# Optimization experiments

Measured on AMD Instinct MI355X. Metric: run time of the kernel, lower is better.

Reference implementation:

```python
import jax, jax.numpy as jnp
import numpy as np

# Config constants (match init_kwargs)
E = 32          # num_experts
K = 4           # num_experts_per_token
G = 4           # num_expert_group
TG = 2          # topk_group
H = 2048        # hidden_size
F = 1024        # moe_intermediate_size
FS = 2048       # shared expert intermediate (moe_intermediate_size * num_shared_experts)
SCALE = 2.0     # routed_scaling_factor
B, S = 2, 1024
N = B * S
CAP = 2 * (N * K // E)


def setup_inputs() -> dict:
    key = jax.random.key(0)
    ks = jax.random.split(key, 9)
    w = 0.02  # init scale for weights
    return {
        "hidden_states": jax.random.normal(ks[0], (B, S, H), jnp.float32),
        "gate_w": jax.random.normal(ks[1], (E, H), jnp.float32) * w,
        "gate_bias": jax.random.normal(ks[2], (E,), jnp.float32) * w,
        "w1": jax.random.normal(ks[3], (E, H, F), jnp.float32) * w,
        "w2": jax.random.normal(ks[4], (E, F, H), jnp.float32) * w,
        "w3": jax.random.normal(ks[5], (E, H, F), jnp.float32) * w,
        "shared_gate": jax.random.normal(ks[6], (H, FS), jnp.float32) * w,
        "shared_up": jax.random.normal(ks[7], (H, FS), jnp.float32) * w,
        "shared_down": jax.random.normal(ks[8], (FS, H), jnp.float32) * w,
    }


def _gate(x, gate_w, gate_bias):
    # x: [N, H] -> (topk_idx [N,K] int32, topk_w [N,K] f32)
    logits = x @ gate_w.T                       # [N, E]
    scores = jax.nn.sigmoid(logits)
    sc = scores + gate_bias                     # scores_for_choice
    n = x.shape[0]
    grp = sc.reshape(n, G, E // G)
    group_scores = jax.lax.top_k(grp, 2)[0].sum(-1)          # [N, G]
    _, gidx = jax.lax.top_k(group_scores, TG)                # [N, TG]
    gmask = jnp.zeros((n, G), sc.dtype).at[jnp.arange(n)[:, None], gidx].set(1.0)
    smask = jnp.repeat(gmask, E // G, axis=1)                # [N, E]
    tmp = jnp.where(smask > 0, sc, 0.0)
    _, topk_idx = jax.lax.top_k(tmp, K)                      # [N, K]
    topk_w = jnp.take_along_axis(scores, topk_idx, axis=1)
    topk_w = topk_w / (topk_w.sum(-1, keepdims=True) + 1e-20)  # renormalize (K>1)
    return topk_idx, topk_w * SCALE


def _moe(x, topk_idx, topk_w, w1, w2, w3):
    # Capacity-based dispatch -> grouped SwiGLU GEMMs -> weighted combine.
    n = x.shape[0]
    flat_e = topk_idx.reshape(-1)                            # [N*K]
    oh = jax.nn.one_hot(flat_e, E, dtype=jnp.int32)
    pos = (jnp.cumsum(oh, axis=0) * oh).sum(-1) - 1          # slot within expert
    keep = pos < CAP
    slot = jnp.where(keep, pos, CAP)                         # CAP -> dropped via mode='drop'
    x_rep = jnp.repeat(x, K, axis=0)                         # [N*K, H]
    buf = jnp.zeros((E, CAP, H), x.dtype).at[flat_e, slot].set(x_rep, mode='drop')
    h = jax.nn.silu(jnp.einsum('ech,ehf->ecf', buf, w1)) * jnp.einsum('ech,ehf->ecf', buf, w3)
    ob = jnp.einsum('ecf,efh->ech', h, w2)                   # [E, CAP, H]
    y = ob[flat_e, jnp.minimum(slot, CAP - 1)]               # [N*K, H]
    y = jnp.where(keep[:, None], y, 0.0)
    return (y.reshape(n, K, H) * topk_w[:, :, None]).sum(1)  # [N, H]


def reference(hidden_states, gate_w, gate_bias, w1, w2, w3, shared_gate, shared_up, shared_down):
    b, s, h = hidden_states.shape
    x = hidden_states.reshape(-1, h)
    topk_idx, topk_w = _gate(x, gate_w, gate_bias)
    out = _moe(x, topk_idx, topk_w, w1, w2, w3)
    shared = (jax.nn.silu(x @ shared_gate) * (x @ shared_up)) @ shared_down
    return (out + shared).reshape(b, s, h)
```

## Files before the change

### kernel.cpp

```cpp
#include <hip/hip_runtime.h>
#include <stdint.h>
#include <math.h>

#define NTOK 2048
#define HDIM 2048
#define FDIM 1024
#define NEXP 32
#define TOPK 4
#define NGRP 4
#define CAP  512

typedef _Float16 f16;
typedef _Float16 half8 __attribute__((ext_vector_type(8)));
typedef _Float16 half2v __attribute__((ext_vector_type(2)));
typedef float f32x4 __attribute__((ext_vector_type(4)));

__device__ __forceinline__ int swz3(int n) { return (n ^ (n >> 2)) & 3; }

__device__ __forceinline__ int expert_off(const int* __restrict__ cnt, int e) {
  int s = 0;
  for (int i = 0; i < e; i++) s += cnt[i];
  return s;
}

__global__ __launch_bounds__(256) void gateconv_kernel(const float* __restrict__ x,
                                                       const float* __restrict__ gw,
                                                       const float* __restrict__ gb,
                                                       int* __restrict__ tidx,
                                                       float* __restrict__ tw,
                                                       f16* __restrict__ xbt) {
  int t = blockIdx.x;
  int tid = threadIdx.x;
  int e = tid >> 3, p = tid & 7;
  const f32x4* xr = (const f32x4*)(x + (size_t)t * HDIM);
  const f32x4* wr = (const f32x4*)(gw + (size_t)e * HDIM);
  float s = 0.f;
  for (int c = 0; c < 64; c++) {
    f32x4 a = xr[p + c * 8], w = wr[p + c * 8];
    s += a[0] * w[0] + a[1] * w[1] + a[2] * w[2] + a[3] * w[3];
  }
  s += __shfl_down(s, 4, 8);
  s += __shfl_down(s, 2, 8);
  s += __shfl_down(s, 1, 8);
  __shared__ float lg[NEXP];
  if (p == 0) lg[e] = s;

  {
    int c8 = tid * 8;
    const float* pp = x + (size_t)t * HDIM + c8;
    f32x4 a = *(const f32x4*)pp;
    f32x4 b = *(const f32x4*)(pp + 4);
    half8 v;
    v[0] = (f16)a[0]; v[1] = (f16)a[1]; v[2] = (f16)a[2]; v[3] = (f16)a[3];
    v[4] = (f16)b[0]; v[5] = (f16)b[1]; v[6] = (f16)b[2]; v[7] = (f16)b[3];
    *(half8*)((char*)xbt + (size_t)(c8 >> 5) * 131072 + t * 64 + (c8 & 31) * 2) = v;
  }

  __syncthreads();
  if (tid == 0) {
    float sc[NEXP], scb[NEXP];
    for (int i = 0; i < NEXP; i++) {
      sc[i] = 1.f / (1.f + expf(-lg[i]));
      scb[i] = sc[i] + gb[i];
    }
    float gs[NGRP];
    for (int g = 0; g < NGRP; g++) {
      float m1 = -1e30f, m2 = -1e30f;
      for (int j = 0; j < 8; j++) {
        float v = scb[g * 8 + j];
        if (v > m1) { m2 = m1; m1 = v; }
        else if (v > m2) m2 = v;
      }
      gs[g] = m1 + m2;
    }
    int g1 = 0; float bv = gs[0];
    for (int g = 1; g < NGRP; g++) if (gs[g] > bv) { bv = gs[g]; g1 = g; }
    int g2 = -1; bv = -1e30f;
    for (int g = 0; g < NGRP; g++) if (g != g1 && gs[g] > bv) { bv = gs[g]; g2 = g; }
    float cand[NEXP];
    for (int i = 0; i < NEXP; i++) {
      int g = i >> 3;
      cand[i] = (g == g1 || g == g2) ? scb[i] : 0.0f;
    }
    int isel[TOPK]; float wsel[TOPK]; float wsum = 0.f;
    bool used[NEXP] = {};
    for (int k = 0; k < TOPK; k++) {
      int best = 0; float bw = -1e30f;
      for (int i = 0; i < NEXP; i++)
        if (!used[i] && cand[i] > bw) { bw = cand[i]; best = i; }
      used[best] = true;
      isel[k] = best;
      wsel[k] = sc[best];
      wsum += wsel[k];
    }
    float inv = 2.0f / (wsum + 1e-20f);
    for (int k = 0; k < TOPK; k++) {
      tidx[t * TOPK + k] = isel[k];
      tw[t * TOPK + k] = wsel[k] * inv;
    }
  }
}

__global__ __launch_bounds__(256) void dispatch_kernel(const int* __restrict__ tidx,
                                                       const float* __restrict__ tw,
                                                       int* __restrict__ tok,
                                                       float* __restrict__ wt,
                                                       int* __restrict__ cnt) {
  int e = blockIdx.x, tid = threadIdx.x, wv = tid >> 6, lane = tid & 63;
  __shared__ int wsum[4];
  __shared__ int sbase;
  if (tid == 0) sbase = 0;
  __syncthreads();
  for (int c = 0; c < (NTOK * TOPK) / 256; c++) {
    int i = c * 256 + tid;
    int fe = tidx[i];
    bool flag = (fe == e);
    unsigned long long b = __ballot(flag ? 1 : 0);
    int lr = __popcll(b & ((1ull << lane) - 1ull));
    if (lane == 0) wsum[wv] = __popcll(b);
    __syncthreads();
    int off = 0;
    for (int w2 = 0; w2 < wv; w2++) off += wsum[w2];
    int tot = wsum[0] + wsum[1] + wsum[2] + wsum[3];
    int base = sbase;
    if (flag) {
      int pos = base + off + lr;
      if (pos < CAP) {
        tok[e * CAP + pos] = i >> 2;
        wt[e * CAP + pos] = tw[i];
      }
    }
    __syncthreads();
    if (tid == 0) sbase = base + tot;
  }
  __syncthreads();
  if (tid == 0) cnt[e] = min(sbase, CAP);
}

__global__ __launch_bounds__(256) void gather_kernel(const f16* __restrict__ xbt,
                                                     const int* __restrict__ tok,
                                                     const int* __restrict__ cnt,
                                                     f16* __restrict__ xg) {
  int bid = blockIdx.x;
  int t = bid & 63, e = bid >> 6;
  int cn = cnt[e];
  int oe = expert_off(cnt, e);
  int tid = threadIdx.x;
  char* dst = (char*)xg + (size_t)oe * 4096 + (size_t)t * cn * 64;
  const char* srcb = (const char*)xbt + (size_t)t * 131072;
  for (int s = tid; s < cn; s += 256) {
    const uint4* sp = (const uint4*)(srcb + (size_t)tok[e * CAP + s] * 64);
    uint4 v0 = sp[0], v1 = sp[1], v2 = sp[2], v3 = sp[3];
    uint4* dp = (uint4*)(dst + s * 64);
    dp[0] = v0; dp[1] = v1; dp[2] = v2; dp[3] = v3;
  }
}

#define SYNC() { asm volatile("s_waitcnt lgkmcnt(0)" ::: "memory"); __builtin_amdgcn_s_barrier(); }

__device__ __forceinline__ void core128(const char* __restrict__ Ab, int tsA, int NKt,
                                        const float* __restrict__ Bb, int ND,
                                        char* lds, f32x4 (&acc)[4][4]) {
  int tid = threadIdx.x, lane = tid & 63, wv = tid >> 6;
  int wn = (wv & 1) * 64;
  int wm = (wv >> 1) * 64;
  int kg = 2 * (lane >> 4) + 8 * wv;
  int n4 = 4 * (lane & 15);
  const float* Br0 = Bb + (size_t)kg * ND + n4;
  const float* Br1 = Bb + (size_t)(kg + 1) * ND + n4;

  unsigned aoff[4];
#pragma unroll
  for (int mf = 0; mf < 4; mf++)
    aoff[mf] = (wm + mf * 16 + (lane & 15)) * 64 + ((lane >> 4) << 4);

  int wo[8];
#pragma unroll
  for (int h = 0; h < 2; h++)
#pragma unroll
    for (int q = 0; q < 4; q++) {
      int n = n4 + 64 * h + q;
      wo[h * 4 + q] = n * 64 + (((kg >> 3) ^ swz3(n)) << 4) + (kg & 7) * 2;
    }

  half8 afA[4], afB[4], bf[4];
  f32x4 E0, E1, E2, E3, O0, O1, O2, O3;

#define LOADB(tt, S0, S1, S2, S3) { size_t _o = (size_t)(tt) * 32 * ND; \
    S0 = *(const f32x4*)(Br0 + _o);      S1 = *(const f32x4*)(Br1 + _o); \
    S2 = *(const f32x4*)(Br0 + _o + 64); S3 = *(const f32x4*)(Br1 + _o + 64); }

#define WRITEB(S0, S1, S2, S3, par) { char* _b = lds + (par) * 8192; \
    _Pragma("unroll") for (int _q = 0; _q < 4; _q++) { \
      half2v _h; _h[0] = (f16)S0[_q]; _h[1] = (f16)S1[_q]; \
      *(half2v*)(_b + wo[_q]) = _h; } \
    _Pragma("unroll") for (int _q = 0; _q < 4; _q++) { \
      half2v _h; _h[0] = (f16)S2[_q]; _h[1] = (f16)S3[_q]; \
      *(half2v*)(_b + wo[4 + _q]) = _h; } }

#define BFREAD(par) { _Pragma("unroll") for (int _f = 0; _f < 4; _f++) { \
      int _n = wn + _f * 16 + (lane & 15); \
      bf[_f] = *(const half8*)(lds + (par) * 8192 + _n * 64 + (((lane >> 4) ^ swz3(_n)) << 4)); } }

#define LOADA(tt, AF) { _Pragma("unroll") for (int _m = 0; _m < 4; _m++) \
      AF[_m] = *(const half8*)(Ab + (size_t)(tt) * tsA + aoff[_m]); }

#define DOMFMA(AF) { _Pragma("unroll") for (int _m = 0; _m < 4; _m++) \
      _Pragma("unroll") for (int _f = 0; _f < 4; _f++) \
        acc[_m][_f] = __builtin_amdgcn_mfma_f32_16x16x32_f16(AF[_m], bf[_f], acc[_m][_f], 0, 0, 0); }

  LOADB(0, E0, E1, E2, E3)
  LOADB(1, O0, O1, O2, O3)
  WRITEB(E0, E1, E2, E3, 0)
  LOADA(0, afA)
  SYNC()

  for (int t = 0; t < NKt; t += 2) {
    BFREAD(0)
    LOADA(t + 1, afB)
    WRITEB(O0, O1, O2, O3, 1)
    if (t + 2 < NKt) LOADB(t + 2, E0, E1, E2, E3)
    DOMFMA(afA)
    SYNC()
    BFREAD(1)
    if (t + 2 < NKt) {
      LOADA(t + 2, afA)
      WRITEB(E0, E1, E2, E3, 0)
      if (t + 3 < NKt) LOADB(t + 3, O0, O1, O2, O3)
    }
    DOMFMA(afB)
    if (t + 2 < NKt) SYNC()
  }

#undef LOADB
#undef WRITEB
#undef BFREAD
#undef LOADA
#undef DOMFMA
}

__global__ __launch_bounds__(256, 3) void fused_up_kernel(
    const f16* __restrict__ xg, const f16* __restrict__ xbt,
    const float* __restrict__ w1, const float* __restrict__ w3,
    const float* __restrict__ sg, const float* __restrict__ su,
    f16* __restrict__ hg, f16* __restrict__ hu,
    f16* __restrict__ hsg, f16* __restrict__ hsu,
    const int* __restrict__ cnt) {
  __shared__ __align__(16) char lds[16384];
  int bid = blockIdx.x;
  int tid = threadIdx.x, lane = tid & 63, wv = tid >> 6;
  int wm = (wv >> 1) * 64, wn = (wv & 1) * 64, koff = (lane >> 4) << 2;

  f32x4 acc[4][4];
#pragma unroll
  for (int mf = 0; mf < 4; mf++)
#pragma unroll
    for (int nf = 0; nf < 4; nf++) acc[mf][nf] = (f32x4){0.f, 0.f, 0.f, 0.f};

  if (bid < 2048) {
    int elo = bid & 7, n = (bid >> 3) & 7, m = (bid >> 6) & 3, ehi = (bid >> 8) & 3, mat = bid >> 10;
    int e = elo + ehi * 8;
    int ce = cnt[e];
    int m0 = m * 128;
    if (m0 >= ce) return;
    int oe = expert_off(cnt, e);
    const char* Ab = (const char*)xg + (size_t)oe * 4096 + m0 * 64;
    const float* B = (mat ? w3 : w1) + (size_t)e * 2048 * 1024 + n * 128;
    core128(Ab, ce * 64, 64, B, 1024, lds, acc);
    char* Hb = (char*)(mat ? hu : hg) + (size_t)oe * 2048;
    size_t kts = (size_t)ce * 64;
#pragma unroll
    for (int mf = 0; mf < 4; mf++)
#pragma unroll
      for (int j = 0; j < 4; j++) {
        int gs = m0 + wm + mf * 16 + koff + j;
        if (gs < ce) {
#pragma unroll
          for (int nf = 0; nf < 4; nf++) {
            int gc = n * 128 + wn + nf * 16 + (lane & 15);
            *(f16*)(Hb + (size_t)(gc >> 5) * kts + gs * 64 + (gc & 31) * 2) = (f16)acc[mf][nf][j];
          }
        }
      }
  } else {
    int b2 = bid - 2048;
    int mat = b2 >> 8, rem = b2 & 255, m = rem >> 4, n = rem & 15;
    int m0 = m * 128;
    const char* Ab = (const char*)xbt + m0 * 64;
    const float* B = (mat ? su : sg) + n * 128;
    core128(Ab, 131072, 64, B, 2048, lds, acc);
    char* Hb = (char*)(mat ? hsu : hsg);
#pragma unroll
    for (int mf = 0; mf < 4; mf++)
#pragma unroll
      for (int j = 0; j < 4; j++) {
        int gs = m0 + wm + mf * 16 + koff + j;
#pragma unroll
        for (int nf = 0; nf < 4; nf++) {
          int gc = n * 128 + wn + nf * 16 + (lane & 15);
          *(f16*)(Hb + (size_t)(gc >> 5) * 131072 + gs * 64 + (gc & 31) * 2) = (f16)acc[mf][nf][j];
        }
      }
  }
}

__global__ __launch_bounds__(256) void combine_kernel(
    const f16* __restrict__ hg, const f16* __restrict__ hu, f16* __restrict__ hbuf,
    const f16* __restrict__ hsg, const f16* __restrict__ hsu, f16* __restrict__ hs) {
  size_t i = ((size_t)blockIdx.x * 256 + threadIdx.x) * 8;
  const f16 *gp, *up;
  f16* op;
  if (i < 8388608) { gp = hg + i; up = hu + i; op = hbuf + i; }
  else { size_t j = i - 8388608; gp = hsg + j; up = hsu + j; op = hs + j; }
  half8 g = *(const half8*)gp;
  half8 u = *(const half8*)up;
  half8 o;
#pragma unroll
  for (int k = 0; k < 8; k++) {
    float gv = (float)g[k];
    float uv = (float)u[k];
    o[k] = (f16)(gv / (1.f + expf(-gv)) * uv);
  }
  *(half8*)op = o;
}

__global__ __launch_bounds__(256, 3) void fused_down_kernel(
    const f16* __restrict__ hbuf, const f16* __restrict__ hs,
    const float* __restrict__ w2, const float* __restrict__ sd,
    float* __restrict__ out, const int* __restrict__ tok,
    const float* __restrict__ wt, const int* __restrict__ cnt) {
  __shared__ __align__(16) char lds[16384];
  int bid = blockIdx.x;
  int tid = threadIdx.x, lane = tid & 63, wv = tid >> 6;
  int wm = (wv >> 1) * 64, wn = (wv & 1) * 64, koff = (lane >> 4) << 2;

  f32x4 acc[4][4];
#pragma unroll
  for (int mf = 0; mf < 4; mf++)
#pragma unroll
    for (int nf = 0; nf < 4; nf++) acc[mf][nf] = (f32x4){0.f, 0.f, 0.f, 0.f};

  if (bid < 2048) {
    int elo = bid & 7, n = (bid >> 3) & 15, m = (bid >> 7) & 3, ehi = (bid >> 9) & 3;
    int e = elo + ehi * 8;
    int ce = cnt[e];
    int m0 = m * 128;
    if (m0 >= ce) return;
    int oe = expert_off(cnt, e);
    const char* Ab = (const char*)hbuf + (size_t)oe * 2048 + m0 * 64;
    const float* B = w2 + (size_t)e * 1024 * 2048 + n * 128;
    core128(Ab, ce * 64, 32, B, 2048, lds, acc);
    const int* tokp = tok + e * CAP;
    const float* wtp = wt + e * CAP;
#pragma unroll
    for (int mf = 0; mf < 4; mf++)
#pragma unroll
      for (int j = 0; j < 4; j++) {
        int gs = m0 + wm + mf * 16 + koff + j;
        if (gs < ce) {
          int tk = tokp[gs];
          float w = wtp[gs];
#pragma unroll
          for (int nf = 0; nf < 4; nf++) {
            int gc = n * 128 + wn + nf * 16 + (lane & 15);
            atomicAdd(out + (size_t)tk * HDIM + gc, acc[mf][nf][j] * w);
          }
        }
      }
  } else {
    int b2 = bid - 2048;
    int m = b2 >> 4, n = b2 & 15;
    int m0 = m * 128;
    const char* Ab = (const char*)hs + m0 * 64;
    const float* B = sd + n * 128;
    core128(Ab, 131072, 64, B, 2048, lds, acc);
#pragma unroll
    for (int mf = 0; mf < 4; mf++)
#pragma unroll
      for (int j = 0; j < 4; j++) {
        int gs = m0 + wm + mf * 16 + koff + j;
#pragma unroll
        for (int nf = 0; nf < 4; nf++) {
          int gc = n * 128 + wn + nf * 16 + (lane & 15);
          atomicAdd(out + (size_t)gs * HDIM + gc, acc[mf][nf][j]);
        }
      }
  }
}

extern "C" void kernel_launch(void* const* d_in, const int* in_sizes, int n_in,
                              void* d_out, int out_size, void* d_ws, size_t ws_size,
                              hipStream_t stream) {
  const float* x  = (const float*)d_in[0];
  const float* gw = (const float*)d_in[1];
  const float* gb = (const float*)d_in[2];
  const float* w1 = (const float*)d_in[3];
  const float* w2 = (const float*)d_in[4];
  const float* w3 = (const float*)d_in[5];
  const float* sg = (const float*)d_in[6];
  const float* su = (const float*)d_in[7];
  const float* sd = (const float*)d_in[8];
  float* out = (float*)d_out;
  char* ws = (char*)d_ws;

  f16*   xbt  = (f16*)(ws);
  f16*   hsg  = (f16*)(ws + 8388608);
  f16*   hsu  = (f16*)(ws + 16777216);
  f16*   hs   = (f16*)(ws + 25165824);
  f16*   hg   = (f16*)(ws + 33554432);
  f16*   hu   = (f16*)(ws + 50331648);
  f16*   xg   = (f16*)(ws + 67108864);
  f16*   hbuf = (f16*)(ws + 67108864);
  int*   tok  = (int*)(ws + 101711872);
  float* wt   = (float*)(ws + 101777408);
  int*   tidx = (int*)(ws + 101842944);
  float* tw   = (float*)(ws + 101875712);
  int*   cnt  = (int*)(ws + 101908480);

  gateconv_kernel<<<2048, 256, 0, stream>>>(x, gw, gb, tidx, tw, xbt);
  dispatch_kernel<<<32, 256, 0, stream>>>(tidx, tw, tok, wt, cnt);
  gather_kernel<<<2048, 256, 0, stream>>>(xbt, tok, cnt, xg);

  fused_up_kernel<<<2560, 256, 0, stream>>>(xg, xbt, w1, w3, sg, su,
                                            hg, hu, hsg, hsu, cnt);
  combine_kernel<<<6144, 256, 0, stream>>>(hg, hu, hbuf, hsg, hsu, hs);

  hipMemsetAsync(out, 0, (size_t)out_size * sizeof(float), stream);
  fused_down_kernel<<<2304, 256, 0, stream>>>(hbuf, hs, w2, sd, out, tok, wt, cnt);
}
```

Measured before the change: 523.4 us.

## Deepen B-tile register prefetch to three stages and unroll K loop by four

```diff
diff --git a/kernel.cpp b/kernel.cpp
--- a/kernel.cpp
+++ b/kernel.cpp
@@ -184,7 +184,10 @@
     }
 
   half8 afA[4], afB[4], bf[4];
-  f32x4 E0, E1, E2, E3, O0, O1, O2, O3;
+  f32x4 A0, A1, A2, A3;
+  f32x4 B0_, B1_, B2_, B3_;
+  f32x4 C0, C1, C2, C3;
+  f32x4 D0, D1, D2, D3;
 
 #define LOADB(tt, S0, S1, S2, S3) { size_t _o = (size_t)(tt) * 32 * ND; \
     S0 = *(const f32x4*)(Br0 + _o);      S1 = *(const f32x4*)(Br1 + _o); \
@@ -209,27 +212,42 @@
       _Pragma("unroll") for (int _f = 0; _f < 4; _f++) \
         acc[_m][_f] = __builtin_amdgcn_mfma_f32_16x16x32_f16(AF[_m], bf[_f], acc[_m][_f], 0, 0, 0); }
 
-  LOADB(0, E0, E1, E2, E3)
-  LOADB(1, O0, O1, O2, O3)
-  WRITEB(E0, E1, E2, E3, 0)
+  LOADB(0, A0, A1, A2, A3)
+  LOADB(1, B0_, B1_, B2_, B3_)
+  LOADB(2, C0, C1, C2, C3)
+  WRITEB(A0, A1, A2, A3, 0)
   LOADA(0, afA)
   SYNC()
 
-  for (int t = 0; t < NKt; t += 2) {
+  for (int t = 0; t < NKt; t += 4) {
     BFREAD(0)
+    WRITEB(B0_, B1_, B2_, B3_, 1)
+    LOADB(t + 3, D0, D1, D2, D3)
+    DOMFMA(afA)
     LOADA(t + 1, afB)
-    WRITEB(O0, O1, O2, O3, 1)
-    if (t + 2 < NKt) LOADB(t + 2, E0, E1, E2, E3)
-    DOMFMA(afA)
     SYNC()
     BFREAD(1)
-    if (t + 2 < NKt) {
-      LOADA(t + 2, afA)
-      WRITEB(E0, E1, E2, E3, 0)
-      if (t + 3 < NKt) LOADB(t + 3, O0, O1, O2, O3)
-    }
+    WRITEB(C0, C1, C2, C3, 0)
+    if (t + 4 < NKt) LOADB(t + 4, A0, A1, A2, A3)
     DOMFMA(afB)
-    if (t + 2 < NKt) SYNC()
+    LOADA(t + 2, afA)
+    SYNC()
+    BFREAD(0)
+    WRITEB(D0, D1, D2, D3, 1)
+    if (t + 5 < NKt) LOADB(t + 5, B0_, B1_, B2_, B3_)
+    DOMFMA(afA)
+    LOADA(t + 3, afB)
+    SYNC()
+    BFREAD(1)
+    if (t + 4 < NKt) {
+      WRITEB(A0, A1, A2, A3, 0)
+      if (t + 6 < NKt) LOADB(t + 6, C0, C1, C2, C3)
+    }
+    DOMFMA(afB)
+    if (t + 4 < NKt) {
+      LOADA(t + 4, afA)
+      SYNC()
+    }
   }
 
 #undef LOADB
@@ -239,7 +257,7 @@
 #undef DOMFMA
 }
 
-__global__ __launch_bounds__(256, 3) void fused_up_kernel(
+__global__ __launch_bounds__(256, 2) void fused_up_kernel(
     const f16* __restrict__ xg, const f16* __restrict__ xbt,
     const float* __restrict__ w1, const float* __restrict__ w3,
     const float* __restrict__ sg, const float* __restrict__ su,
@@ -324,7 +342,7 @@
   *(half8*)op = o;
 }
 
-__global__ __launch_bounds__(256, 3) void fused_down_kernel(
+__global__ __launch_bounds__(256, 2) void fused_down_kernel(
     const f16* __restrict__ hbuf, const f16* __restrict__ hs,
     const float* __restrict__ w2, const float* __restrict__ sd,
     float* __restrict__ out, const int* __restrict__ tok,
```

Result: slower. 540.3 us (+3.2%).
